# Kernel tuning notes

Hardware: AMD Instinct MI355X
Metric: run time of the kernel (lower is better)

## Reference

```python
import jax, jax.numpy as jnp
import numpy as np

EMBED_DIM = 1024
NUM_HEADS = 16
HEAD_DIM = EMBED_DIM // NUM_HEADS
B, S = 4, 2048


def setup_inputs() -> dict:
    key = jax.random.key(0)
    ks = jax.random.split(key, 11)
    scale = 1.0 / np.sqrt(EMBED_DIM)
    def lin(k):
        kw, kb = jax.random.split(k)
        W = jax.random.uniform(kw, (EMBED_DIM, EMBED_DIM), jnp.float32, -scale, scale)
        b = jax.random.uniform(kb, (EMBED_DIM,), jnp.float32, -scale, scale)
        return W, b
    Wq, bq = lin(ks[0]); Wk, bk = lin(ks[1]); Wv, bv = lin(ks[2]); Wo, bo = lin(ks[3])
    return {
        "query": jax.random.normal(ks[4], (B, S, EMBED_DIM), jnp.float32),
        "key": jax.random.normal(ks[5], (B, S, EMBED_DIM), jnp.float32),
        "value": jax.random.normal(ks[6], (B, S, EMBED_DIM), jnp.float32),
        "Wq": Wq, "bq": bq, "Wk": Wk, "bk": bk, "Wv": Wv, "bv": bv, "Wo": Wo, "bo": bo,
    }


def reference(query, key, value, Wq, bq, Wk, bk, Wv, bv, Wo, bo):
    Bz, Sz, E = query.shape
    H, Dh = NUM_HEADS, HEAD_DIM
    # projections -> [B, H, S, Dh]
    q = (query @ Wq + bq).reshape(Bz, Sz, H, Dh).transpose(0, 2, 1, 3)
    k = (key @ Wk + bk).reshape(Bz, Sz, H, Dh).transpose(0, 2, 1, 3)
    v = (value @ Wv + bv).reshape(Bz, Sz, H, Dh).transpose(0, 2, 1, 3)
    scores = jnp.einsum('bhsd,bhtd->bhst', q, k) / jnp.sqrt(jnp.asarray(Dh, q.dtype))
    attn = jax.nn.softmax(scores, axis=-1)  # dropout is identity in eval mode
    out = jnp.einsum('bhst,bhtd->bhsd', attn, v)  # [B,H,S,Dh]
    out = out.transpose(0, 2, 1, 3).reshape(Bz, Sz, E)
    out = out @ Wo + bo
    return out, attn
```

## Files before the change

kernel.cpp:

```cpp
#include <hip/hip_runtime.h>
#include <stdint.h>


using bf16x8 = __attribute__((ext_vector_type(8))) short;
using f32x4  = __attribute__((ext_vector_type(4))) float;
using u16x4  = __attribute__((ext_vector_type(4))) unsigned short;
using u64x2  = __attribute__((ext_vector_type(2))) unsigned long long;

#define MFMA_BF16 __builtin_amdgcn_mfma_f32_16x16x32_bf16

__device__ __forceinline__ unsigned short f2bf(float x) {
    unsigned int u = __builtin_bit_cast(unsigned int, x);
    u = (u + 0x7FFFu + ((u >> 16) & 1u)) >> 16;
    return (unsigned short)u;
}
__device__ __forceinline__ float bf2f(unsigned short u) {
    return __builtin_bit_cast(float, (unsigned int)u << 16);
}
__device__ __forceinline__ float exp2_fast(float x) {
    float r; asm("v_exp_f32 %0, %1" : "=v"(r) : "v"(x)); return r;
}
__device__ __forceinline__ float log2_fast(float x) {
    float r; asm("v_log_f32 %0, %1" : "=v"(r) : "v"(x)); return r;
}
__device__ __forceinline__ void gload_lds16(const unsigned short* g, bf16x8* l) {
    __builtin_amdgcn_global_load_lds(
        (const __attribute__((address_space(1))) unsigned int*)(g),
        (__attribute__((address_space(3))) unsigned int*)(l), 16, 0, 0);
}

__global__ __launch_bounds__(256) void wtrans_kernel(
    const float* __restrict__ w0, const float* __restrict__ w1,
    const float* __restrict__ w2, const float* __restrict__ w3,
    unsigned short* __restrict__ Wt)
{
    __shared__ float tile[64][65];
    const float* src = (blockIdx.z == 0) ? w0 : (blockIdx.z == 1) ? w1 :
                       (blockIdx.z == 2) ? w2 : w3;
    unsigned short* dst = Wt + (size_t)blockIdx.z * (1u << 20);
    const int k0 = blockIdx.x * 64, n0 = blockIdx.y * 64;
    const int tid = threadIdx.x;
#pragma unroll
    for (int i = 0; i < 16; ++i) {
        int idx = i * 256 + tid;
        int kk = idx >> 6, nn = idx & 63;
        tile[kk][nn] = src[(size_t)(k0 + kk) * 1024 + n0 + nn];
    }
    __syncthreads();
#pragma unroll
    for (int i = 0; i < 16; ++i) {
        int idx = i * 256 + tid;
        int nn = idx >> 6, kk = idx & 63;
        dst[(size_t)(n0 + nn) * 1024 + k0 + kk] = f2bf(tile[kk][nn]);
    }
}

template<bool A_BF16, int OUT_MODE>
__global__ __launch_bounds__(256) void gemm_kernel(
    const void* __restrict__ Aip, const unsigned short* __restrict__ Bt,
    const float* __restrict__ bias, void* __restrict__ Cp, float prescale)
{
    __shared__ bf16x8 Alds[1024];
    __shared__ bf16x8 Blds[1024];
    const int tid = threadIdx.x;
    const int lane = tid & 63;
    const int w = tid >> 6;
    const int wm = w >> 1, wn = w & 1;
    const int m0 = blockIdx.x * 128, n0 = blockIdx.y * 128;
    const int r16 = lane & 15, g = lane >> 4;

    f32x4 acc[4][4] = {};

    for (int kt = 0; kt < 16; ++kt) {
        const int k0 = kt * 64;
#pragma unroll
        for (int issue = 0; issue < 4; ++issue) {
            int s = issue * 256 + tid;
            int row = s >> 3, cc = (s & 7) ^ (row & 7);
            gload_lds16(Bt + (size_t)(n0 + row) * 1024 + k0 + cc * 8,
                        &Blds[issue * 256 + w * 64]);
        }
        if constexpr (A_BF16) {
            const unsigned short* A = (const unsigned short*)Aip;
#pragma unroll
            for (int issue = 0; issue < 4; ++issue) {
                int s = issue * 256 + tid;
                int row = s >> 3, cc = (s & 7) ^ (row & 7);
                gload_lds16(A + (size_t)(m0 + row) * 1024 + k0 + cc * 8,
                            &Alds[issue * 256 + w * 64]);
            }
        } else {
            const float* A = (const float*)Aip;
#pragma unroll
            for (int i = 0; i < 4; ++i) {
                int c = i * 256 + tid;
                int row = c >> 3, cc = c & 7;
                const float* sp = A + (size_t)(m0 + row) * 1024 + k0 + cc * 8;
                float4 v0 = *(const float4*)sp;
                float4 v1 = *(const float4*)(sp + 4);
                bf16x8 v;
                v[0] = f2bf(v0.x); v[1] = f2bf(v0.y); v[2] = f2bf(v0.z); v[3] = f2bf(v0.w);
                v[4] = f2bf(v1.x); v[5] = f2bf(v1.y); v[6] = f2bf(v1.z); v[7] = f2bf(v1.w);
                Alds[row * 8 + (cc ^ (row & 7))] = v;
            }
        }
        __syncthreads();
#pragma unroll
        for (int ks = 0; ks < 2; ++ks) {
            bf16x8 af[4], bfr[4];
#pragma unroll
            for (int mf = 0; mf < 4; ++mf) {
                int row = wm * 64 + mf * 16 + r16;
                af[mf] = Alds[row * 8 + ((ks * 4 + g) ^ (row & 7))];
            }
#pragma unroll
            for (int nf = 0; nf < 4; ++nf) {
                int row = wn * 64 + nf * 16 + r16;
                bfr[nf] = Blds[row * 8 + ((ks * 4 + g) ^ (row & 7))];
            }
#pragma unroll
            for (int mf = 0; mf < 4; ++mf)
#pragma unroll
                for (int nf = 0; nf < 4; ++nf)
                    acc[mf][nf] = MFMA_BF16(af[mf], bfr[nf], acc[mf][nf], 0, 0, 0);
        }
        __syncthreads();
    }

#pragma unroll
    for (int nf = 0; nf < 4; ++nf) {
        const int n = n0 + wn * 64 + nf * 16 + r16;
        const float bv = bias[n];
#pragma unroll
        for (int mf = 0; mf < 4; ++mf) {
            const int mb = m0 + wm * 64 + mf * 16 + g * 4;
            if constexpr (OUT_MODE == 2) {
                float* C = (float*)Cp;
#pragma unroll
                for (int r = 0; r < 4; ++r)
                    C[(size_t)(mb + r) * 1024 + n] = acc[mf][nf][r] + bv;
            } else if constexpr (OUT_MODE == 0) {
                unsigned short* C = (unsigned short*)Cp;
                const int h = n >> 6, d = n & 63;
#pragma unroll
                for (int r = 0; r < 4; ++r) {
                    int m = mb + r;
                    int b = m >> 11, s2 = m & 2047;
                    C[((((size_t)b * 16 + h) * 2048 + s2) << 6) + d] =
                        f2bf((acc[mf][nf][r] + bv) * prescale);
                }
            } else {
                unsigned short* C = (unsigned short*)Cp;
                const int h = n >> 6, d = n & 63;
                const int b = mb >> 11, s2 = mb & 2047;
                u16x4 pk;
#pragma unroll
                for (int r = 0; r < 4; ++r) pk[r] = f2bf(acc[mf][nf][r] + bv);
                *(u16x4*)(C + (((size_t)b * 16 + h) * 64 + d) * 2048 + s2) = pk;
            }
        }
    }
}

__global__ __launch_bounds__(256) void attn_kernel(
    const unsigned short* __restrict__ Q,
    const unsigned short* __restrict__ K,
    const unsigned short* __restrict__ VT,
    float* __restrict__ attn,
    unsigned short* __restrict__ ctx)
{
    __shared__ bf16x8 k_buf[2][64 * 8];
    __shared__ bf16x8 v_buf[2][64 * 8];
    __shared__ unsigned long long p_buf[64 * 16];

    const int tid = threadIdx.x;
    const int lane = tid & 63;
    const int w = tid >> 6;
    const int L = blockIdx.x;
    const int xcd = L & 7, j = L >> 3;
    const int qt = j & 31;
    const int bh = ((j >> 5) << 3) | xcd;
    const int r16 = lane & 15, g = lane >> 4;

    const unsigned short* Kb = K + (size_t)bh * 2048 * 64;
    const unsigned short* Vb = VT + (size_t)bh * 64 * 2048;

    const int row0 = tid >> 3, cc0 = tid & 7;
    const int row1 = row0 + 32;
    const int kslot0 = row0 * 8 + (cc0 ^ (row0 & 7));
    const int kslot1 = row1 * 8 + (cc0 ^ (row1 & 7));

    const int qrow = w * 16 + r16;
    const unsigned short* qptr = Q + ((size_t)bh * 2048 + (size_t)qt * 64 + qrow) * 64 + g * 8;
    const bf16x8 qf0 = *(const bf16x8*)(qptr);
    const bf16x8 qf1 = *(const bf16x8*)(qptr + 32);

    k_buf[0][kslot0] = *(const bf16x8*)(Kb + (size_t)row0 * 64 + cc0 * 8);
    k_buf[0][kslot1] = *(const bf16x8*)(Kb + (size_t)row1 * 64 + cc0 * 8);
    bf16x8 pf0 = *(const bf16x8*)(Kb + 4096 + (size_t)row0 * 64 + cc0 * 8);
    bf16x8 pf1 = *(const bf16x8*)(Kb + 4096 + (size_t)row1 * 64 + cc0 * 8);
    __syncthreads();

    float l4[4] = {0.f, 0.f, 0.f, 0.f};
#pragma unroll 2
    for (int kt = 0; kt < 32; ++kt) {
        const int cur = kt & 1;
        bf16x8 nn0, nn1;
        if (kt + 2 < 32) {
            const unsigned short* src = Kb + (size_t)(kt + 2) * 4096;
            nn0 = *(const bf16x8*)(src + (size_t)row0 * 64 + cc0 * 8);
            nn1 = *(const bf16x8*)(src + (size_t)row1 * 64 + cc0 * 8);
        }
#pragma unroll
        for (int kf = 0; kf < 4; ++kf) {
            const int row = kf * 16 + r16;
            f32x4 t = {};
            t = MFMA_BF16(k_buf[cur][row * 8 + ((0 + g) ^ (row & 7))], qf0, t, 0, 0, 0);
            t = MFMA_BF16(k_buf[cur][row * 8 + ((4 + g) ^ (row & 7))], qf1, t, 0, 0, 0);
#pragma unroll
            for (int r = 0; r < 4; ++r) l4[r] += exp2_fast(t[r]);
        }
        if (kt + 1 < 32) {
            k_buf[cur ^ 1][kslot0] = pf0;
            k_buf[cur ^ 1][kslot1] = pf1;
        }
        __syncthreads();
        pf0 = nn0;
        pf1 = nn1;
    }
    float l_acc = (l4[0] + l4[1]) + (l4[2] + l4[3]);
    l_acc += __shfl_xor(l_acc, 16, 64);
    l_acc += __shfl_xor(l_acc, 32, 64);
    const float lg2invl = -log2_fast(l_acc);

    {
        bf16x8 a0 = *(const bf16x8*)(Kb + (size_t)row0 * 64 + cc0 * 8);
        bf16x8 a1 = *(const bf16x8*)(Kb + (size_t)row1 * 64 + cc0 * 8);
        bf16x8 b0 = *(const bf16x8*)(Vb + (size_t)row0 * 2048 + cc0 * 8);
        bf16x8 b1 = *(const bf16x8*)(Vb + (size_t)row1 * 2048 + cc0 * 8);
        k_buf[0][kslot0] = a0; k_buf[0][kslot1] = a1;
        v_buf[0][kslot0] = b0; v_buf[0][kslot1] = b1;
    }
    __syncthreads();

    float* attn_tile = attn + ((size_t)bh * 2048 + (size_t)qt * 64) * 2048;
    const f32x4 cinit = {lg2invl, lg2invl, lg2invl, lg2invl};

    f32x4 oacc[4] = {};
    for (int kt = 0; kt < 32; ++kt) {
        const int cur = kt & 1;
        bf16x8 nk0, nk1, nv0, nv1;
        if (kt != 31) {
            const unsigned short* ksrc = Kb + (size_t)(kt + 1) * 64 * 64;
            const unsigned short* vsrc = Vb + (size_t)(kt + 1) * 64;
            nk0 = *(const bf16x8*)(ksrc + (size_t)row0 * 64 + cc0 * 8);
            nk1 = *(const bf16x8*)(ksrc + (size_t)row1 * 64 + cc0 * 8);
            nv0 = *(const bf16x8*)(vsrc + (size_t)row0 * 2048 + cc0 * 8);
            nv1 = *(const bf16x8*)(vsrc + (size_t)row1 * 2048 + cc0 * 8);
        }
#pragma unroll
        for (int kf = 0; kf < 4; ++kf) {
            const int row = kf * 16 + r16;
            f32x4 t = cinit;
            t = MFMA_BF16(k_buf[cur][row * 8 + ((0 + g) ^ (row & 7))], qf0, t, 0, 0, 0);
            t = MFMA_BF16(k_buf[cur][row * 8 + ((4 + g) ^ (row & 7))], qf1, t, 0, 0, 0);
            u16x4 pk;
#pragma unroll
            for (int r = 0; r < 4; ++r) pk[r] = f2bf(exp2_fast(t[r]));
            const int c = 2 * kf + (g >> 1);
            p_buf[qrow * 16 + ((c ^ (qrow & 7)) << 1) + (g & 1)] =
                __builtin_bit_cast(unsigned long long, pk);
        }
#pragma unroll
        for (int i = 0; i < 2; ++i)
#pragma unroll
            for (int jj = 0; jj < 2; ++jj) {
                const int srow = w * 16 + i * 8 + (lane >> 3);
                const int col0 = jj * 32 + (lane & 7) * 4;
                const int c = col0 >> 3, half = (col0 >> 2) & 1;
                unsigned long long praw =
                    p_buf[srow * 16 + ((c ^ (srow & 7)) << 1) + half];
                u16x4 pk = __builtin_bit_cast(u16x4, praw);
                f32x4 pv = {bf2f(pk[0]), bf2f(pk[1]), bf2f(pk[2]), bf2f(pk[3])};
                __builtin_nontemporal_store(
                    pv, (f32x4*)(attn_tile + (size_t)srow * 2048 + kt * 64 + col0));
            }
#pragma unroll
        for (int ks = 0; ks < 2; ++ks) {
            const int cs = (ks * 4 + g) ^ (qrow & 7);
            u64x2 praw2 = {p_buf[qrow * 16 + cs * 2], p_buf[qrow * 16 + cs * 2 + 1]};
            bf16x8 a = __builtin_bit_cast(bf16x8, praw2);
#pragma unroll
            for (int df = 0; df < 4; ++df) {
                const int rowv = df * 16 + r16;
                oacc[df] = MFMA_BF16(a, v_buf[cur][rowv * 8 + ((ks * 4 + g) ^ (rowv & 7))],
                                     oacc[df], 0, 0, 0);
            }
        }
        if (kt != 31) {
            k_buf[cur ^ 1][kslot0] = nk0; k_buf[cur ^ 1][kslot1] = nk1;
            v_buf[cur ^ 1][kslot0] = nv0; v_buf[cur ^ 1][kslot1] = nv1;
        }
        __syncthreads();
    }

    const int b = bh >> 4, h = bh & 15;
#pragma unroll
    for (int df = 0; df < 4; ++df) {
        int d = df * 16 + r16;
#pragma unroll
        for (int r = 0; r < 4; ++r) {
            int s2 = qt * 64 + w * 16 + g * 4 + r;
            ctx[((size_t)b * 2048 + s2) * 1024 + h * 64 + d] = f2bf(oacc[df][r]);
        }
    }
}

extern "C" void kernel_launch(void* const* d_in, const int* in_sizes, int n_in,
                              void* d_out, int out_size, void* d_ws, size_t ws_size,
                              hipStream_t stream)
{
    (void)in_sizes; (void)n_in; (void)out_size; (void)ws_size;
    const float* query = (const float*)d_in[0];
    const float* key_  = (const float*)d_in[1];
    const float* value = (const float*)d_in[2];
    const float* Wq = (const float*)d_in[3];
    const float* bq = (const float*)d_in[4];
    const float* Wk = (const float*)d_in[5];
    const float* bk = (const float*)d_in[6];
    const float* Wv = (const float*)d_in[7];
    const float* bv = (const float*)d_in[8];
    const float* Wo = (const float*)d_in[9];
    const float* bo = (const float*)d_in[10];

    char* ws = (char*)d_ws;
    unsigned short* Wt  = (unsigned short*)(ws);
    unsigned short* qb  = (unsigned short*)(ws + ((size_t)8  << 20));
    unsigned short* kb  = (unsigned short*)(ws + ((size_t)24 << 20));
    unsigned short* vtb = (unsigned short*)(ws + ((size_t)40 << 20));
    unsigned short* ctx = (unsigned short*)(ws + ((size_t)56 << 20));
    float* outp = (float*)d_out;
    float* attn = outp + (size_t)4 * 2048 * 1024;

    const float qscale = 0.125f * 1.44269504089f;

    wtrans_kernel<<<dim3(16, 16, 4), 256, 0, stream>>>(Wq, Wk, Wv, Wo, Wt);
    gemm_kernel<false, 0><<<dim3(64, 8), 256, 0, stream>>>(query, Wt,              bq, qb,  qscale);
    gemm_kernel<false, 0><<<dim3(64, 8), 256, 0, stream>>>(key_,  Wt + (1u << 20), bk, kb,  1.0f);
    gemm_kernel<false, 1><<<dim3(64, 8), 256, 0, stream>>>(value, Wt + (2u << 20), bv, vtb, 1.0f);
    attn_kernel<<<dim3(2048), 256, 0, stream>>>(qb, kb, vtb, attn, ctx);
    gemm_kernel<true, 2><<<dim3(64, 8), 256, 0, stream>>>(ctx, Wt + (3u << 20), bo, outp, 1.0f);
}
```

Baseline: 368.8 us.

## Process two query tiles per attention block to share K/V tile loads

Each attention workgroup now handles two adjacent 64-row query tiles against the same K/V stream, so each K and V tile staged in shared memory is used twice. The grid is halved accordingly. The intent is to cut global K/V traffic and LDS staging per unit of work. In exchange it adds register pressure from doubled accumulators and query fragments, and fewer blocks may lower occupancy. The kernel likely remains bound by the large fp32 attention-matrix stores.

After: 381.0 us. 1.03x slower.

```diff
diff --git a/kernel.cpp b/kernel.cpp
--- a/kernel.cpp
+++ b/kernel.cpp
@@ -178,8 +178,9 @@
     const int w = tid >> 6;
     const int L = blockIdx.x;
     const int xcd = L & 7, j = L >> 3;
-    const int qt = j & 31;
-    const int bh = ((j >> 5) << 3) | xcd;
+    const int pair = j & 15;
+    const int qtA = pair * 2, qtB = pair * 2 + 1;
+    const int bh = ((j >> 4) << 3) | xcd;
     const int r16 = lane & 15, g = lane >> 4;
 
     const unsigned short* Kb = K + (size_t)bh * 2048 * 64;
@@ -191,9 +192,14 @@
     const int kslot1 = row1 * 8 + (cc0 ^ (row1 & 7));
 
     const int qrow = w * 16 + r16;
-    const unsigned short* qptr = Q + ((size_t)bh * 2048 + (size_t)qt * 64 + qrow) * 64 + g * 8;
-    const bf16x8 qf0 = *(const bf16x8*)(qptr);
-    const bf16x8 qf1 = *(const bf16x8*)(qptr + 32);
+    const unsigned short* qptrA =
+        Q + ((size_t)bh * 2048 + (size_t)qtA * 64 + qrow) * 64 + g * 8;
+    const bf16x8 qfA0 = *(const bf16x8*)(qptrA);
+    const bf16x8 qfA1 = *(const bf16x8*)(qptrA + 32);
+    const unsigned short* qptrB =
+        Q + ((size_t)bh * 2048 + (size_t)qtB * 64 + qrow) * 64 + g * 8;
+    const bf16x8 qfB0 = *(const bf16x8*)(qptrB);
+    const bf16x8 qfB1 = *(const bf16x8*)(qptrB + 32);
 
     k_buf[0][kslot0] = *(const bf16x8*)(Kb + (size_t)row0 * 64 + cc0 * 8);
     k_buf[0][kslot1] = *(const bf16x8*)(Kb + (size_t)row1 * 64 + cc0 * 8);
@@ -201,7 +207,8 @@
     bf16x8 pf1 = *(const bf16x8*)(Kb + 4096 + (size_t)row1 * 64 + cc0 * 8);
     __syncthreads();
 
-    float l4[4] = {0.f, 0.f, 0.f, 0.f};
+    float l4A[4] = {0.f, 0.f, 0.f, 0.f};
+    float l4B[4] = {0.f, 0.f, 0.f, 0.f};
 #pragma unroll 2
     for (int kt = 0; kt < 32; ++kt) {
         const int cur = kt & 1;
@@ -214,11 +221,18 @@
 #pragma unroll
         for (int kf = 0; kf < 4; ++kf) {
             const int row = kf * 16 + r16;
-            f32x4 t = {};
-            t = MFMA_BF16(k_buf[cur][row * 8 + ((0 + g) ^ (row & 7))], qf0, t, 0, 0, 0);
-            t = MFMA_BF16(k_buf[cur][row * 8 + ((4 + g) ^ (row & 7))], qf1, t, 0, 0, 0);
-#pragma unroll
-            for (int r = 0; r < 4; ++r) l4[r] += exp2_fast(t[r]);
+            const bf16x8 k0v = k_buf[cur][row * 8 + ((0 + g) ^ (row & 7))];
+            const bf16x8 k1v = k_buf[cur][row * 8 + ((4 + g) ^ (row & 7))];
+            f32x4 tA = {};
+            tA = MFMA_BF16(k0v, qfA0, tA, 0, 0, 0);
+            tA = MFMA_BF16(k1v, qfA1, tA, 0, 0, 0);
+#pragma unroll
+            for (int r = 0; r < 4; ++r) l4A[r] += exp2_fast(tA[r]);
+            f32x4 tB = {};
+            tB = MFMA_BF16(k0v, qfB0, tB, 0, 0, 0);
+            tB = MFMA_BF16(k1v, qfB1, tB, 0, 0, 0);
+#pragma unroll
+            for (int r = 0; r < 4; ++r) l4B[r] += exp2_fast(tB[r]);
         }
         if (kt + 1 < 32) {
             k_buf[cur ^ 1][kslot0] = pf0;
@@ -228,10 +242,14 @@
         pf0 = nn0;
         pf1 = nn1;
     }
-    float l_acc = (l4[0] + l4[1]) + (l4[2] + l4[3]);
-    l_acc += __shfl_xor(l_acc, 16, 64);
-    l_acc += __shfl_xor(l_acc, 32, 64);
-    const float lg2invl = -log2_fast(l_acc);
+    float lA = (l4A[0] + l4A[1]) + (l4A[2] + l4A[3]);
+    lA += __shfl_xor(lA, 16, 64);
+    lA += __shfl_xor(lA, 32, 64);
+    const float lg2invlA = -log2_fast(lA);
+    float lB = (l4B[0] + l4B[1]) + (l4B[2] + l4B[3]);
+    lB += __shfl_xor(lB, 16, 64);
+    lB += __shfl_xor(lB, 32, 64);
+    const float lg2invlB = -log2_fast(lB);
 
     {
         bf16x8 a0 = *(const bf16x8*)(Kb + (size_t)row0 * 64 + cc0 * 8);
@@ -243,10 +261,13 @@
     }
     __syncthreads();
 
-    float* attn_tile = attn + ((size_t)bh * 2048 + (size_t)qt * 64) * 2048;
-    const f32x4 cinit = {lg2invl, lg2invl, lg2invl, lg2invl};
-
-    f32x4 oacc[4] = {};
+    float* attn_tileA = attn + ((size_t)bh * 2048 + (size_t)qtA * 64) * 2048;
+    float* attn_tileB = attn + ((size_t)bh * 2048 + (size_t)qtB * 64) * 2048;
+    const f32x4 cinitA = {lg2invlA, lg2invlA, lg2invlA, lg2invlA};
+    const f32x4 cinitB = {lg2invlB, lg2invlB, lg2invlB, lg2invlB};
+
+    f32x4 oaccA[4] = {};
+    f32x4 oaccB[4] = {};
     for (int kt = 0; kt < 32; ++kt) {
         const int cur = kt & 1;
         bf16x8 nk0, nk1, nv0, nv1;
@@ -261,9 +282,9 @@
 #pragma unroll
         for (int kf = 0; kf < 4; ++kf) {
             const int row = kf * 16 + r16;
-            f32x4 t = cinit;
-            t = MFMA_BF16(k_buf[cur][row * 8 + ((0 + g) ^ (row & 7))], qf0, t, 0, 0, 0);
-            t = MFMA_BF16(k_buf[cur][row * 8 + ((4 + g) ^ (row & 7))], qf1, t, 0, 0, 0);
+            f32x4 t = cinitA;
+            t = MFMA_BF16(k_buf[cur][row * 8 + ((0 + g) ^ (row & 7))], qfA0, t, 0, 0, 0);
+            t = MFMA_BF16(k_buf[cur][row * 8 + ((4 + g) ^ (row & 7))], qfA1, t, 0, 0, 0);
             u16x4 pk;
 #pragma unroll
             for (int r = 0; r < 4; ++r) pk[r] = f2bf(exp2_fast(t[r]));
@@ -283,7 +304,7 @@
                 u16x4 pk = __builtin_bit_cast(u16x4, praw);
                 f32x4 pv = {bf2f(pk[0]), bf2f(pk[1]), bf2f(pk[2]), bf2f(pk[3])};
                 __builtin_nontemporal_store(
-                    pv, (f32x4*)(attn_tile + (size_t)srow * 2048 + kt * 64 + col0));
+                    pv, (f32x4*)(attn_tileA + (size_t)srow * 2048 + kt * 64 + col0));
             }
 #pragma unroll
         for (int ks = 0; ks < 2; ++ks) {
@@ -293,8 +314,47 @@
 #pragma unroll
             for (int df = 0; df < 4; ++df) {
                 const int rowv = df * 16 + r16;
-                oacc[df] = MFMA_BF16(a, v_buf[cur][rowv * 8 + ((ks * 4 + g) ^ (rowv & 7))],
-                                     oacc[df], 0, 0, 0);
+                oaccA[df] = MFMA_BF16(a, v_buf[cur][rowv * 8 + ((ks * 4 + g) ^ (rowv & 7))],
+                                      oaccA[df], 0, 0, 0);
+            }
+        }
+#pragma unroll
+        for (int kf = 0; kf < 4; ++kf) {
+            const int row = kf * 16 + r16;
+            f32x4 t = cinitB;
+            t = MFMA_BF16(k_buf[cur][row * 8 + ((0 + g) ^ (row & 7))], qfB0, t, 0, 0, 0);
+            t = MFMA_BF16(k_buf[cur][row * 8 + ((4 + g) ^ (row & 7))], qfB1, t, 0, 0, 0);
+            u16x4 pk;
+#pragma unroll
+            for (int r = 0; r < 4; ++r) pk[r] = f2bf(exp2_fast(t[r]));
+            const int c = 2 * kf + (g >> 1);
+            p_buf[qrow * 16 + ((c ^ (qrow & 7)) << 1) + (g & 1)] =
+                __builtin_bit_cast(unsigned long long, pk);
+        }
+#pragma unroll
+        for (int i = 0; i < 2; ++i)
+#pragma unroll
+            for (int jj = 0; jj < 2; ++jj) {
+                const int srow = w * 16 + i * 8 + (lane >> 3);
+                const int col0 = jj * 32 + (lane & 7) * 4;
+                const int c = col0 >> 3, half = (col0 >> 2) & 1;
+                unsigned long long praw =
+                    p_buf[srow * 16 + ((c ^ (srow & 7)) << 1) + half];
+                u16x4 pk = __builtin_bit_cast(u16x4, praw);
+                f32x4 pv = {bf2f(pk[0]), bf2f(pk[1]), bf2f(pk[2]), bf2f(pk[3])};
+                __builtin_nontemporal_store(
+                    pv, (f32x4*)(attn_tileB + (size_t)srow * 2048 + kt * 64 + col0));
+            }
+#pragma unroll
+        for (int ks = 0; ks < 2; ++ks) {
+            const int cs = (ks * 4 + g) ^ (qrow & 7);
+            u64x2 praw2 = {p_buf[qrow * 16 + cs * 2], p_buf[qrow * 16 + cs * 2 + 1]};
+            bf16x8 a = __builtin_bit_cast(bf16x8, praw2);
+#pragma unroll
+            for (int df = 0; df < 4; ++df) {
+                const int rowv = df * 16 + r16;
+                oaccB[df] = MFMA_BF16(a, v_buf[cur][rowv * 8 + ((ks * 4 + g) ^ (rowv & 7))],
+                                      oaccB[df], 0, 0, 0);
             }
         }
         if (kt != 31) {
@@ -310,8 +370,10 @@
         int d = df * 16 + r16;
 #pragma unroll
         for (int r = 0; r < 4; ++r) {
-            int s2 = qt * 64 + w * 16 + g * 4 + r;
-            ctx[((size_t)b * 2048 + s2) * 1024 + h * 64 + d] = f2bf(oacc[df][r]);
+            int s2A = qtA * 64 + w * 16 + g * 4 + r;
+            ctx[((size_t)b * 2048 + s2A) * 1024 + h * 64 + d] = f2bf(oaccA[df][r]);
+            int s2B = qtB * 64 + w * 16 + g * 4 + r;
+            ctx[((size_t)b * 2048 + s2B) * 1024 + h * 64 + d] = f2bf(oaccB[df][r]);
         }
     }
 }
@@ -348,6 +410,6 @@
     gemm_kernel<false, 0><<<dim3(64, 8), 256, 0, stream>>>(query, Wt,              bq, qb,  qscale);
     gemm_kernel<false, 0><<<dim3(64, 8), 256, 0, stream>>>(key_,  Wt + (1u << 20), bk, kb,  1.0f);
     gemm_kernel<false, 1><<<dim3(64, 8), 256, 0, stream>>>(value, Wt + (2u << 20), bv, vtb, 1.0f);
-    attn_kernel<<<dim3(2048), 256, 0, stream>>>(qb, kb, vtb, attn, ctx);
+    attn_kernel<<<dim3(1024), 256, 0, stream>>>(qb, kb, vtb, attn, ctx);
     gemm_kernel<true, 2><<<dim3(64, 8), 256, 0, stream>>>(ctx, Wt + (3u << 20), bo, outp, 1.0f);
 }
```
